# Kernel optimization log

Measured on AMD Instinct MI355X. Metric: run time of the kernel, lower is better.

The kernel has to match this reference:

```python
import jax, jax.numpy as jnp
import numpy as np

N_NODES = 50000
N_EDGES = 800000
N_GRAPHS = 512
D = 128
NUM_GIN_LAYERS = 4
BN_EPS = 1e-5


def setup_inputs() -> dict:
    key = jax.random.key(0)
    ks = jax.random.split(key, 10)
    h = jax.random.normal(ks[0], (N_NODES, D), dtype=jnp.float32)
    src = jax.random.randint(ks[1], (N_EDGES,), 0, N_NODES, dtype=jnp.int32)
    dst = jax.random.randint(ks[2], (N_EDGES,), 0, N_NODES, dtype=jnp.int32)
    graph_id = jnp.sort(jax.random.randint(ks[3], (N_NODES,), 0, N_GRAPHS, dtype=jnp.int32))
    scale = 1.0 / np.sqrt(D)
    W1s = jax.random.normal(ks[4], (NUM_GIN_LAYERS, D, D), dtype=jnp.float32) * scale
    W2s = jax.random.normal(ks[5], (NUM_GIN_LAYERS, D, D), dtype=jnp.float32) * scale
    bn1_g = jnp.ones((NUM_GIN_LAYERS, D), jnp.float32)
    bn1_b = jnp.zeros((NUM_GIN_LAYERS, D), jnp.float32)
    bn2_g = jnp.ones((NUM_GIN_LAYERS, D), jnp.float32)
    bn2_b = jnp.zeros((NUM_GIN_LAYERS, D), jnp.float32)
    pred_W = jax.random.normal(ks[6], (NUM_GIN_LAYERS + 1, D, D), dtype=jnp.float32) * scale
    pred_b = jnp.zeros((NUM_GIN_LAYERS + 1, D), jnp.float32)
    return {"h": h, "src": src, "dst": dst, "graph_id": graph_id,
            "W1s": W1s, "W2s": W2s, "bn1_g": bn1_g, "bn1_b": bn1_b,
            "bn2_g": bn2_g, "bn2_b": bn2_b, "pred_W": pred_W, "pred_b": pred_b}


def _batch_norm(x, gamma, beta):
    # training-mode BN over the node axis
    mean = jnp.mean(x, axis=0)
    var = jnp.var(x, axis=0)
    return (x - mean) * jax.lax.rsqrt(var + BN_EPS) * gamma + beta


def reference(h, src, dst, graph_id, W1s, W2s, bn1_g, bn1_b, bn2_g, bn2_b, pred_W, pred_b):
    n = h.shape[0]
    hidden_rep = [h]
    for i in range(NUM_GIN_LAYERS):
        # GINConv, eps=0: (1+eps)*h + sum over in-neighbors (scatter-sum over edges)
        agg = jax.ops.segment_sum(h[src], dst, num_segments=n)
        z = h + agg
        # two-layer MLP: Linear(no bias) -> BN -> ReLU -> Linear(no bias)
        z = jax.nn.relu(_batch_norm(z @ W1s[i], bn1_g[i], bn1_b[i]))
        z = z @ W2s[i]
        # outer BN + ReLU
        h = jax.nn.relu(_batch_norm(z, bn2_g[i], bn2_b[i]))
        hidden_rep.append(h)
    # graph readout: per-graph max pool over each layer's representation,
    # then per-layer linear prediction summed (dropout is identity in eval)
    score = jnp.zeros((N_GRAPHS, pred_W.shape[-1]), h.dtype)
    for i, hr in enumerate(hidden_rep):
        pooled = jax.ops.segment_max(hr, graph_id, num_segments=N_GRAPHS,
                                     indices_are_sorted=True)
        score = score + pooled @ pred_W[i] + pred_b[i]
    return score
```

## Files before the change

### kernel.cpp

```cpp
#include <hip/hip_runtime.h>

#define N_NODES 50000
#define N_EDGES 800000
#define N_GRAPHS 512
#define DIM 128
#define NLAYERS 4
#define BN_EPS 1e-5f
#define NTILE (N_NODES / 16)
#define POIS ((int)0xAAAAAAAA)
#define NREP 8

#define NBUCK 80
#define CAPB 12288
#define EPB 1600
#define NBIN 500

typedef unsigned short u16;
typedef float f32x2 __attribute__((ext_vector_type(2)));
typedef float f32x4 __attribute__((ext_vector_type(4)));
typedef short bf16x8 __attribute__((ext_vector_type(8)));

__device__ __forceinline__ short f2bs(float f) {
    union { float f; unsigned u; } v; v.f = f;
    unsigned r = v.u + 0x7FFFu + ((v.u >> 16) & 1u);
    return (short)(r >> 16);
}
__device__ __forceinline__ float bu2f(unsigned u) {
    union { unsigned u; float f; } v; v.u = u << 16;
    return v.f;
}
__device__ __forceinline__ unsigned packbf(float x, float y) {
    return ((unsigned)(u16)f2bs(y) << 16) | (unsigned)(u16)f2bs(x);
}

__device__ __forceinline__ void foldbn(const float* __restrict__ st,
                                       const float* __restrict__ gamma,
                                       const float* __restrict__ beta,
                                       float* absm, int tid) {
    if (tid < 128) {
        float s = 0.f, sq = 0.f;
#pragma unroll
        for (int j = 0; j < NREP; j++) {
            s += st[j * 256 + tid];
            sq += st[j * 256 + 128 + tid];
        }
        float mean = s * (1.f / N_NODES);
        float var = sq * (1.f / N_NODES) - mean * mean;
        float a = gamma[tid] * rsqrtf(var + BN_EPS);
        absm[tid] = a;
        absm[DIM + tid] = beta[tid] - mean * a;
    }
}

__global__ __launch_bounds__(256) void k_prepbin(const float* __restrict__ h,
                                                 const float* __restrict__ W1s,
                                                 const float* __restrict__ W2s,
                                                 const int* __restrict__ gid,
                                                 const int* __restrict__ src,
                                                 const int* __restrict__ dst,
                                                 unsigned* __restrict__ hb,
                                                 short* __restrict__ wt,
                                                 int* __restrict__ gs, int* __restrict__ ge,
                                                 unsigned* __restrict__ eb,
                                                 int* __restrict__ gcur) {
    __shared__ int hist[NBUCK], base[NBUCK], lcur[NBUCK];
    int bid = blockIdx.x, tid = threadIdx.x;
    if (bid >= 6250) {
        int bbid = bid - 6250;
        if (tid < NBUCK) hist[tid] = 0;
        __syncthreads();
        int e0 = bbid * EPB;
        unsigned rec[7]; int rb[7];
#pragma unroll
        for (int k = 0; k < 7; k++) {
            int idx = tid + k * 256;
            rb[k] = -1;
            if (idx < EPB) {
                int s = src[e0 + idx], d = dst[e0 + idx];
                rec[k] = ((unsigned)d << 16) | (unsigned)s;
                int x = d / 6250;
                int sub = (d - x * 6250) / 625;
                rb[k] = x + 8 * sub;
                atomicAdd(&hist[rb[k]], 1);
            }
        }
        __syncthreads();
        if (tid < NBUCK) {
            int old = atomicAdd(&gcur[tid], hist[tid]);
            base[tid] = old - POIS;
            lcur[tid] = 0;
        }
        __syncthreads();
#pragma unroll
        for (int k = 0; k < 7; k++) {
            if (rb[k] >= 0) {
                int p = atomicAdd(&lcur[rb[k]], 1);
                eb[rb[k] * CAPB + base[rb[k]] + p] = rec[k];
            }
        }
        return;
    }
    int gtid = bid * 256 + tid;
    {
        f32x4 v = *(const f32x4*)(h + gtid * 4);
        uint2 pp;
        pp.x = packbf(v.x, v.y);
        pp.y = packbf(v.z, v.w);
        *(uint2*)(hb + gtid * 2) = pp;
    }
    if (gtid < 8 * 16384) {
        int m = gtid >> 14, r = gtid & 16383, n = r >> 7, k = r & 127;
        const float* W = (m < 4) ? (W1s + m * 16384) : (W2s + (m - 4) * 16384);
        wt[gtid] = f2bs(W[k * DIM + n]);
    }
    if (gtid < N_NODES) {
        int g = gid[gtid];
        if (gtid == 0 || gid[gtid - 1] != g) gs[g] = gtid;
        if (gtid == N_NODES - 1 || gid[gtid + 1] != g) ge[g] = gtid + 1;
    }
}

__global__ __launch_bounds__(256) void k_fillpool0(const unsigned* __restrict__ eb,
                                                   const int* __restrict__ gcur,
                                                   int* __restrict__ begA,
                                                   int* __restrict__ endA,
                                                   u16* __restrict__ eix,
                                                   const float* __restrict__ h,
                                                   const int* __restrict__ gs,
                                                   const int* __restrict__ ge,
                                                   float* __restrict__ pool4) {
    __shared__ int hist[625], begL[625], sm[256];
    __shared__ f32x2 psm[256];
    int bid = blockIdx.x, tid = threadIdx.x;
    if (bid < NBUCK) {
        int x = bid & 7, sub = bid >> 3;
        int n0 = x * 6250 + sub * 625;
        int mybase = 0, mycnt = 0;
        for (int r = 0; r < NBUCK; r++) {
            int c = gcur[r] - POIS;
            int rx = r & 7, rs = r >> 3;
            if (rx < x || (rx == x && rs < sub)) mybase += c;
            if (r == bid) mycnt = c;
        }
        for (int i = tid; i < 625; i += 256) hist[i] = 0;
        __syncthreads();
        const unsigned* my = eb + bid * CAPB;
        for (int i = tid; i < mycnt; i += 256) {
            int dl = (int)(my[i] >> 16) - n0;
            atomicAdd(&hist[dl], 1);
        }
        __syncthreads();
        int carry = 0;
        for (int c = 0; c < 3; c++) {
            int idx = c * 256 + tid;
            int v = (idx < 625) ? hist[idx] : 0;
            int xv = v;
            sm[tid] = xv; __syncthreads();
#pragma unroll
            for (int d = 1; d < 256; d <<= 1) {
                int y = (tid >= d) ? sm[tid - d] : 0;
                __syncthreads();
                sm[tid] = xv = xv + y;
                __syncthreads();
            }
            if (idx < 625) begL[idx] = mybase + carry + xv - v;
            int ct = sm[255];
            __syncthreads();
            carry += ct;
        }
        __syncthreads();
        for (int i = tid; i < 625; i += 256) {
            int b = begL[i];
            begA[n0 + i] = b;
            endA[n0 + i] = b + hist[i];
        }
        __syncthreads();
        for (int i = tid; i < mycnt; i += 256) {
            unsigned rc = my[i];
            int dl = (int)(rc >> 16) - n0;
            int p = atomicAdd(&begL[dl], 1);
            eix[p] = (u16)(rc & 0xFFFFu);
        }
        return;
    }
    int pb = bid - NBUCK;
    int g = pb >> 2, sub = pb & 3;
    int c2 = (tid & 63) * 2, ro = tid >> 6;
    int beg = gs[g], end = ge[g];
    f32x2 mx = (f32x2){-3.402823e38f, -3.402823e38f};
    if (beg >= 0 && end <= N_NODES) {
        for (int r = beg + sub * 4 + ro; r < end; r += 16) {
            f32x2 v = *(const f32x2*)(h + r * DIM + c2);
            mx.x = fmaxf(mx.x, v.x);
            mx.y = fmaxf(mx.y, v.y);
        }
    }
    psm[tid] = mx;
    __syncthreads();
    if (ro == 0) {
        f32x2 m0 = psm[tid], m1 = psm[tid + 64], m2 = psm[tid + 128], m3 = psm[tid + 192];
        m0.x = fmaxf(fmaxf(m0.x, m1.x), fmaxf(m2.x, m3.x));
        m0.y = fmaxf(fmaxf(m0.y, m1.y), fmaxf(m2.y, m3.y));
        *(f32x2*)(pool4 + pb * DIM + c2) = m0;
    }
}

template <bool XF>
__global__ __launch_bounds__(256) void k_gather(const unsigned* __restrict__ hp,
                                                const int* __restrict__ begA,
                                                const int* __restrict__ endA,
                                                const u16* __restrict__ eix,
                                                const float* __restrict__ absg,
                                                unsigned* __restrict__ Za) {
    int node = blockIdx.x * 4 + (threadIdx.x >> 6);
    int lane = threadIdx.x & 63;
    float a0 = 1.f, a1 = 1.f, b0 = 0.f, b1 = 0.f;
    if (XF) {
        a0 = absg[2 * lane]; a1 = absg[2 * lane + 1];
        b0 = absg[DIM + 2 * lane]; b1 = absg[DIM + 2 * lane + 1];
    }
#define TX(w, rx, ry)                                     \
    {                                                     \
        float _x = bu2f((w) & 0xffffu), _y = bu2f((w) >> 16); \
        if (XF) {                                         \
            _x = fmaxf(a0 * _x + b0, 0.f);                \
            _y = fmaxf(a1 * _y + b1, 0.f);                \
        }                                                 \
        rx += _x; ry += _y;                               \
    }
    float ax = 0.f, ay = 0.f;
    TX(hp[node * 64 + lane], ax, ay);
    int beg = begA[node];
    int end = endA[node];
    int e = beg;
    for (; e + 8 <= end; e += 8) {
        int s0 = eix[e], s1 = eix[e + 1], s2 = eix[e + 2], s3 = eix[e + 3];
        int s4 = eix[e + 4], s5 = eix[e + 5], s6 = eix[e + 6], s7 = eix[e + 7];
        unsigned w0 = hp[s0 * 64 + lane], w1 = hp[s1 * 64 + lane];
        unsigned w2 = hp[s2 * 64 + lane], w3 = hp[s3 * 64 + lane];
        unsigned w4 = hp[s4 * 64 + lane], w5 = hp[s5 * 64 + lane];
        unsigned w6 = hp[s6 * 64 + lane], w7 = hp[s7 * 64 + lane];
        TX(w0, ax, ay); TX(w1, ax, ay); TX(w2, ax, ay); TX(w3, ax, ay);
        TX(w4, ax, ay); TX(w5, ax, ay); TX(w6, ax, ay); TX(w7, ax, ay);
    }
    for (; e < end; e++) {
        unsigned ww = hp[eix[e] * 64 + lane];
        TX(ww, ax, ay);
    }
#undef TX
    Za[node * 64 + lane] = packbf(ax, ay);
}

template <bool XF>
__global__ __launch_bounds__(256, 2) void k_gemm(const unsigned* __restrict__ X,
                                                 const short* __restrict__ wt,
                                                 const float* __restrict__ statsPrev,
                                                 const float* __restrict__ gamma,
                                                 const float* __restrict__ beta,
                                                 unsigned* __restrict__ OUT,
                                                 float* __restrict__ statsDst) {
    __shared__ float tbuf[4][16][68];
    __shared__ float absm[256];
    __shared__ float smst[256];
    const int tid = threadIdx.x, bid = blockIdx.x;
    const int lane = tid & 63, wid = tid >> 6;
    const int ln15 = lane & 15, q = lane >> 4;
    float (*buf)[68] = tbuf[wid];

    bf16x8 bfr[8][4];
#pragma unroll
    for (int tl = 0; tl < 8; tl++)
#pragma unroll
        for (int s = 0; s < 4; s++)
            bfr[tl][s] = *(const bf16x8*)(wt + (tl * 16 + ln15) * DIM + s * 32 + q * 8);

    if (XF) foldbn(statsPrev, gamma, beta, absm, tid);
    smst[tid] = 0.f;
    __syncthreads();

    float sac[8], qac[8];
#pragma unroll
    for (int t = 0; t < 8; t++) { sac[t] = 0.f; qac[t] = 0.f; }

    f32x4 aA[4], aB[4], bA[4], bB[4];
    if (XF) {
#pragma unroll
        for (int s = 0; s < 4; s++) {
            int k0 = s * 32 + q * 8;
            aA[s] = *(const f32x4*)(absm + k0);
            aB[s] = *(const f32x4*)(absm + k0 + 4);
            bA[s] = *(const f32x4*)(absm + DIM + k0);
            bB[s] = *(const f32x4*)(absm + DIM + k0 + 4);
        }
    }

    for (int tile = bid * 4 + wid; tile < NTILE; tile += gridDim.x * 4) {
        const unsigned* xr = X + (tile * 16 + ln15) * 64;
        bf16x8 afr[4];
        if constexpr (!XF) {
#pragma unroll
            for (int s = 0; s < 4; s++)
                afr[s] = *(const bf16x8*)(xr + s * 16 + q * 4);
        } else {
#pragma unroll
            for (int s = 0; s < 4; s++) {
                uint4 wv = *(const uint4*)(xr + s * 16 + q * 4);
                float v0 = fmaxf(aA[s].x * bu2f(wv.x & 0xffffu) + bA[s].x, 0.f);
                float v1 = fmaxf(aA[s].y * bu2f(wv.x >> 16) + bA[s].y, 0.f);
                float v2 = fmaxf(aA[s].z * bu2f(wv.y & 0xffffu) + bA[s].z, 0.f);
                float v3 = fmaxf(aA[s].w * bu2f(wv.y >> 16) + bA[s].w, 0.f);
                float v4 = fmaxf(aB[s].x * bu2f(wv.z & 0xffffu) + bB[s].x, 0.f);
                float v5 = fmaxf(aB[s].y * bu2f(wv.z >> 16) + bB[s].y, 0.f);
                float v6 = fmaxf(aB[s].z * bu2f(wv.w & 0xffffu) + bB[s].z, 0.f);
                float v7 = fmaxf(aB[s].w * bu2f(wv.w >> 16) + bB[s].w, 0.f);
                bf16x8 a;
                a[0] = f2bs(v0); a[1] = f2bs(v1); a[2] = f2bs(v2); a[3] = f2bs(v3);
                a[4] = f2bs(v4); a[5] = f2bs(v5); a[6] = f2bs(v6); a[7] = f2bs(v7);
                afr[s] = a;
            }
        }
        f32x4 acc[8];
#pragma unroll
        for (int t = 0; t < 8; t++) acc[t] = (f32x4){0.f, 0.f, 0.f, 0.f};
#pragma unroll
        for (int s = 0; s < 4; s++) {
#pragma unroll
            for (int t = 0; t < 8; t++)
                acc[t] = __builtin_amdgcn_mfma_f32_16x16x32_bf16(afr[s], bfr[t][s], acc[t], 0, 0, 0);
        }
#pragma unroll
        for (int t = 0; t < 8; t++) {
            float s_l = 0.f, q_l = 0.f;
#pragma unroll
            for (int r = 0; r < 4; r++) {
                float v = acc[t][r];
                s_l += v;
                q_l += v * v;
            }
            s_l += __shfl_xor(s_l, 16); s_l += __shfl_xor(s_l, 32);
            q_l += __shfl_xor(q_l, 16); q_l += __shfl_xor(q_l, 32);
            sac[t] += s_l;
            qac[t] += q_l;
        }
#pragma unroll
        for (int ch = 0; ch < 2; ch++) {
#pragma unroll
            for (int t2 = 0; t2 < 4; t2++) {
                int t = ch * 4 + t2;
#pragma unroll
                for (int r = 0; r < 4; r++)
                    buf[q * 4 + r][t2 * 16 + ln15] = acc[t][r];
            }
#pragma unroll
            for (int rr = 0; rr < 4; rr++) {
                int lr = rr * 4 + q;
                f32x4 v = *(const f32x4*)&buf[lr][ln15 * 4];
                uint2 pp;
                pp.x = packbf(v.x, v.y);
                pp.y = packbf(v.z, v.w);
                *(uint2*)(OUT + (tile * 16 + lr) * 64 + ch * 32 + ln15 * 2) = pp;
            }
        }
    }
    if (lane < 16) {
#pragma unroll
        for (int t = 0; t < 8; t++) {
            atomicAdd(&smst[t * 16 + ln15], sac[t]);
            atomicAdd(&smst[128 + t * 16 + ln15], qac[t]);
        }
    }
    __syncthreads();
    atomicAdd(statsDst + (bid & (NREP - 1)) * 256 + tid, smst[tid]);
}

__global__ __launch_bounds__(256) void k_pool(const unsigned* __restrict__ Zr,
                                              const float* __restrict__ stats,
                                              const float* __restrict__ gamma,
                                              const float* __restrict__ beta,
                                              const int* __restrict__ gs,
                                              const int* __restrict__ ge,
                                              float* __restrict__ pool4,
                                              float* __restrict__ absg) {
    __shared__ float absm[256];
    __shared__ f32x2 psm[256];
    int bid = blockIdx.x, tid = threadIdx.x;
    int g = bid >> 2, sub = bid & 3;
    foldbn(stats, gamma, beta, absm, tid);
    __syncthreads();
    if (bid == 0) absg[tid] = absm[tid];
    int ci = tid & 63, ro = tid >> 6;
    int beg = gs[g], end = ge[g];
    f32x2 a = *(const f32x2*)(absm + ci * 2);
    f32x2 b = *(const f32x2*)(absm + DIM + ci * 2);
    f32x2 mx = (f32x2){-3.402823e38f, -3.402823e38f};
    if (beg >= 0 && end <= N_NODES) {
        for (int r = beg + sub * 4 + ro; r < end; r += 16) {
            unsigned w = Zr[r * 64 + ci];
            float vx = fmaxf(a.x * bu2f(w & 0xffffu) + b.x, 0.f);
            float vy = fmaxf(a.y * bu2f(w >> 16) + b.y, 0.f);
            mx.x = fmaxf(mx.x, vx);
            mx.y = fmaxf(mx.y, vy);
        }
    }
    psm[tid] = mx;
    __syncthreads();
    if (ro == 0) {
        f32x2 m0 = psm[tid], m1 = psm[tid + 64], m2 = psm[tid + 128], m3 = psm[tid + 192];
        m0.x = fmaxf(fmaxf(m0.x, m1.x), fmaxf(m2.x, m3.x));
        m0.y = fmaxf(fmaxf(m0.y, m1.y), fmaxf(m2.y, m3.y));
        *(f32x2*)(pool4 + bid * DIM + ci * 2) = m0;
    }
}

__global__ __launch_bounds__(640) void k_readout(const float* __restrict__ pool4,
                                                 const float* __restrict__ predW,
                                                 const float* __restrict__ predb,
                                                 float* __restrict__ out) {
    __shared__ float pl[5][DIM];
    __shared__ float ps[5][DIM];
    int g = blockIdx.x, t = threadIdx.x;
    int l = t >> 7, c = t & 127;
    {
        const float* p = pool4 + l * (N_GRAPHS * 4 * DIM) + g * 4 * DIM + c;
        float m = fmaxf(fmaxf(p[0], p[DIM]), fmaxf(p[2 * DIM], p[3 * DIM]));
        pl[l][c] = m;
    }
    __syncthreads();
    float acc = 0.f;
    const float* W = predW + l * DIM * DIM;
    const float* prow = pl[l];
#pragma unroll 8
    for (int k = 0; k < DIM; k++) acc += prow[k] * W[k * DIM + c];
    ps[l][c] = acc;
    __syncthreads();
    if (t < DIM) {
        float s = 0.f;
#pragma unroll
        for (int ll = 0; ll < 5; ll++) s += ps[ll][c] + predb[ll * DIM + c];
        out[g * DIM + c] = s;
    }
}

extern "C" void kernel_launch(void* const* d_in, const int* in_sizes, int n_in,
                              void* d_out, int out_size, void* d_ws, size_t ws_size,
                              hipStream_t stream) {
    const float* h_in = (const float*)d_in[0];
    const int* src = (const int*)d_in[1];
    const int* dst = (const int*)d_in[2];
    const int* gid = (const int*)d_in[3];
    const float* W1s = (const float*)d_in[4];
    const float* W2s = (const float*)d_in[5];
    const float* bn1g = (const float*)d_in[6];
    const float* bn1b = (const float*)d_in[7];
    const float* bn2g = (const float*)d_in[8];
    const float* bn2b = (const float*)d_in[9];
    const float* predW = (const float*)d_in[10];
    const float* predb = (const float*)d_in[11];

    char* ws = (char*)d_ws;
    unsigned* hb = (unsigned*)(ws);
    unsigned* Za = (unsigned*)(ws + 12800000);
    unsigned* Yb = (unsigned*)(ws + 25600000);
    unsigned* Zr = (unsigned*)(ws + 38400000);
    short* wt = (short*)(ws + 51200000);
    float* stats = (float*)(ws + 51462144);
    float* pool4 = (float*)(ws + 51527680);
    int* begA = (int*)(ws + 56770560);
    int* endA = (int*)(ws + 56970560);
    u16* eix = (u16*)(ws + 57372800);
    int* gs = (int*)(ws + 60572800);
    int* ge = (int*)(ws + 60574848);
    float* absg = (float*)(ws + 60576896);
    unsigned* eb = (unsigned*)(ws + 25600000);
    int* gcur = (int*)(ws + 25600000 + 8388608);
    float* out = (float*)d_out;

    const int PSTRIDE = N_GRAPHS * 4 * DIM;

    k_prepbin<<<6750, 256, 0, stream>>>(h_in, W1s, W2s, gid, src, dst, hb, wt, gs, ge, eb, gcur);
    k_fillpool0<<<NBUCK + 2048, 256, 0, stream>>>(eb, gcur, begA, endA, eix, h_in, gs, ge, pool4);

    for (int l = 0; l < NLAYERS; l++) {
        if (l == 0)
            k_gather<false><<<12500, 256, 0, stream>>>(hb, begA, endA, eix, absg, Za);
        else
            k_gather<true><<<12500, 256, 0, stream>>>(Zr, begA, endA, eix, absg, Za);
        k_gemm<false><<<512, 256, 0, stream>>>(Za, wt + l * 16384, nullptr, nullptr, nullptr,
                                               Yb, stats + (l * 2) * (NREP * 256));
        k_gemm<true><<<512, 256, 0, stream>>>(Yb, wt + (4 + l) * 16384,
                                              stats + (l * 2) * (NREP * 256), bn1g + l * DIM,
                                              bn1b + l * DIM, Zr,
                                              stats + (l * 2 + 1) * (NREP * 256));
        k_pool<<<2048, 256, 0, stream>>>(Zr, stats + (l * 2 + 1) * (NREP * 256),
                                         bn2g + l * DIM, bn2b + l * DIM, gs, ge,
                                         pool4 + (l + 1) * PSTRIDE, absg);
    }
    k_readout<<<512, 640, 0, stream>>>(pool4, predW, predb, out);
}
```

Measured before the change: 488.3 us.

## Fuse per-layer max-pool into next layer's gather kernel and prefetch GEMM input tiles

The max-pool for layers 0-2 now runs inside the following layer's gather kernel, through extra blocks in one launch. This removes three kernel launches and the absg round trip, and each gather block recomputes the BN fold itself. The GEMM kernels get a fixed tile assignment with register double-buffering, loading the next tile's A fragment before computing the current one to hide global load latency. The stats buffer also moves to a new workspace offset.

```diff
diff --git a/kernel.cpp b/kernel.cpp
--- a/kernel.cpp
+++ b/kernel.cpp
@@ -205,30 +205,18 @@
     }
 }
 
-template <bool XF>
-__global__ __launch_bounds__(256) void k_gather(const unsigned* __restrict__ hp,
-                                                const int* __restrict__ begA,
-                                                const int* __restrict__ endA,
-                                                const u16* __restrict__ eix,
-                                                const float* __restrict__ absg,
-                                                unsigned* __restrict__ Za) {
+__global__ __launch_bounds__(256) void k_gather0(const unsigned* __restrict__ hp,
+                                                 const int* __restrict__ begA,
+                                                 const int* __restrict__ endA,
+                                                 const u16* __restrict__ eix,
+                                                 unsigned* __restrict__ Za) {
     int node = blockIdx.x * 4 + (threadIdx.x >> 6);
     int lane = threadIdx.x & 63;
-    float a0 = 1.f, a1 = 1.f, b0 = 0.f, b1 = 0.f;
-    if (XF) {
-        a0 = absg[2 * lane]; a1 = absg[2 * lane + 1];
-        b0 = absg[DIM + 2 * lane]; b1 = absg[DIM + 2 * lane + 1];
-    }
-#define TX(w, rx, ry)                                     \
-    {                                                     \
-        float _x = bu2f((w) & 0xffffu), _y = bu2f((w) >> 16); \
-        if (XF) {                                         \
-            _x = fmaxf(a0 * _x + b0, 0.f);                \
-            _y = fmaxf(a1 * _y + b1, 0.f);                \
-        }                                                 \
-        rx += _x; ry += _y;                               \
-    }
     float ax = 0.f, ay = 0.f;
+#define TX(w, rx, ry)                                         \
+    {                                                         \
+        rx += bu2f((w) & 0xffffu); ry += bu2f((w) >> 16);     \
+    }
     TX(hp[node * 64 + lane], ax, ay);
     int beg = begA[node];
     int end = endA[node];
@@ -245,6 +233,82 @@
     }
     for (; e < end; e++) {
         unsigned ww = hp[eix[e] * 64 + lane];
+        TX(ww, ax, ay);
+    }
+#undef TX
+    Za[node * 64 + lane] = packbf(ax, ay);
+}
+
+__global__ __launch_bounds__(256) void k_poolgather(const unsigned* __restrict__ Zr,
+                                                    const float* __restrict__ stats,
+                                                    const float* __restrict__ gamma,
+                                                    const float* __restrict__ beta,
+                                                    const int* __restrict__ gs,
+                                                    const int* __restrict__ ge,
+                                                    float* __restrict__ pool4,
+                                                    const int* __restrict__ begA,
+                                                    const int* __restrict__ endA,
+                                                    const u16* __restrict__ eix,
+                                                    unsigned* __restrict__ Za) {
+    __shared__ float absm[256];
+    __shared__ f32x2 psm[256];
+    int bid = blockIdx.x, tid = threadIdx.x;
+    foldbn(stats, gamma, beta, absm, tid);
+    __syncthreads();
+    if (bid < 2048) {
+        int g = bid >> 2, sub = bid & 3;
+        int ci = tid & 63, ro = tid >> 6;
+        int beg = gs[g], end = ge[g];
+        f32x2 a = *(const f32x2*)(absm + ci * 2);
+        f32x2 b = *(const f32x2*)(absm + DIM + ci * 2);
+        f32x2 mx = (f32x2){-3.402823e38f, -3.402823e38f};
+        if (beg >= 0 && end <= N_NODES) {
+            for (int r = beg + sub * 4 + ro; r < end; r += 16) {
+                unsigned w = Zr[r * 64 + ci];
+                float vx = fmaxf(a.x * bu2f(w & 0xffffu) + b.x, 0.f);
+                float vy = fmaxf(a.y * bu2f(w >> 16) + b.y, 0.f);
+                mx.x = fmaxf(mx.x, vx);
+                mx.y = fmaxf(mx.y, vy);
+            }
+        }
+        psm[tid] = mx;
+        __syncthreads();
+        if (ro == 0) {
+            f32x2 m0 = psm[tid], m1 = psm[tid + 64], m2 = psm[tid + 128], m3 = psm[tid + 192];
+            m0.x = fmaxf(fmaxf(m0.x, m1.x), fmaxf(m2.x, m3.x));
+            m0.y = fmaxf(fmaxf(m0.y, m1.y), fmaxf(m2.y, m3.y));
+            *(f32x2*)(pool4 + bid * DIM + ci * 2) = m0;
+        }
+        return;
+    }
+    int node = (bid - 2048) * 4 + (tid >> 6);
+    int lane = tid & 63;
+    float a0 = absm[2 * lane], a1 = absm[2 * lane + 1];
+    float b0 = absm[DIM + 2 * lane], b1 = absm[DIM + 2 * lane + 1];
+#define TX(w, rx, ry)                                         \
+    {                                                         \
+        float _x = bu2f((w) & 0xffffu), _y = bu2f((w) >> 16); \
+        _x = fmaxf(a0 * _x + b0, 0.f);                        \
+        _y = fmaxf(a1 * _y + b1, 0.f);                        \
+        rx += _x; ry += _y;                                   \
+    }
+    float ax = 0.f, ay = 0.f;
+    TX(Zr[node * 64 + lane], ax, ay);
+    int beg = begA[node];
+    int end = endA[node];
+    int e = beg;
+    for (; e + 8 <= end; e += 8) {
+        int s0 = eix[e], s1 = eix[e + 1], s2 = eix[e + 2], s3 = eix[e + 3];
+        int s4 = eix[e + 4], s5 = eix[e + 5], s6 = eix[e + 6], s7 = eix[e + 7];
+        unsigned w0 = Zr[s0 * 64 + lane], w1 = Zr[s1 * 64 + lane];
+        unsigned w2 = Zr[s2 * 64 + lane], w3 = Zr[s3 * 64 + lane];
+        unsigned w4 = Zr[s4 * 64 + lane], w5 = Zr[s5 * 64 + lane];
+        unsigned w6 = Zr[s6 * 64 + lane], w7 = Zr[s7 * 64 + lane];
+        TX(w0, ax, ay); TX(w1, ax, ay); TX(w2, ax, ay); TX(w3, ax, ay);
+        TX(w4, ax, ay); TX(w5, ax, ay); TX(w6, ax, ay); TX(w7, ax, ay);
+    }
+    for (; e < end; e++) {
+        unsigned ww = Zr[eix[e] * 64 + lane];
         TX(ww, ax, ay);
     }
 #undef TX
@@ -294,25 +358,37 @@
         }
     }
 
-    for (int tile = bid * 4 + wid; tile < NTILE; tile += gridDim.x * 4) {
+    int tile = bid + 512 * wid;
+    uint4 wv[4];
+    if (tile < NTILE) {
         const unsigned* xr = X + (tile * 16 + ln15) * 64;
+#pragma unroll
+        for (int s = 0; s < 4; s++) wv[s] = *(const uint4*)(xr + s * 16 + q * 4);
+    }
+    while (tile < NTILE) {
+        int nt = tile + 2048;
+        uint4 nwv[4];
+        if (nt < NTILE) {
+            const unsigned* xr2 = X + (nt * 16 + ln15) * 64;
+#pragma unroll
+            for (int s = 0; s < 4; s++) nwv[s] = *(const uint4*)(xr2 + s * 16 + q * 4);
+        }
         bf16x8 afr[4];
         if constexpr (!XF) {
 #pragma unroll
-            for (int s = 0; s < 4; s++)
-                afr[s] = *(const bf16x8*)(xr + s * 16 + q * 4);
+            for (int s = 0; s < 4; s++) afr[s] = *(bf16x8*)&wv[s];
         } else {
 #pragma unroll
             for (int s = 0; s < 4; s++) {
-                uint4 wv = *(const uint4*)(xr + s * 16 + q * 4);
-                float v0 = fmaxf(aA[s].x * bu2f(wv.x & 0xffffu) + bA[s].x, 0.f);
-                float v1 = fmaxf(aA[s].y * bu2f(wv.x >> 16) + bA[s].y, 0.f);
-                float v2 = fmaxf(aA[s].z * bu2f(wv.y & 0xffffu) + bA[s].z, 0.f);
-                float v3 = fmaxf(aA[s].w * bu2f(wv.y >> 16) + bA[s].w, 0.f);
-                float v4 = fmaxf(aB[s].x * bu2f(wv.z & 0xffffu) + bB[s].x, 0.f);
-                float v5 = fmaxf(aB[s].y * bu2f(wv.z >> 16) + bB[s].y, 0.f);
-                float v6 = fmaxf(aB[s].z * bu2f(wv.w & 0xffffu) + bB[s].z, 0.f);
-                float v7 = fmaxf(aB[s].w * bu2f(wv.w >> 16) + bB[s].w, 0.f);
+                uint4 w4v = wv[s];
+                float v0 = fmaxf(aA[s].x * bu2f(w4v.x & 0xffffu) + bA[s].x, 0.f);
+                float v1 = fmaxf(aA[s].y * bu2f(w4v.x >> 16) + bA[s].y, 0.f);
+                float v2 = fmaxf(aA[s].z * bu2f(w4v.y & 0xffffu) + bA[s].z, 0.f);
+                float v3 = fmaxf(aA[s].w * bu2f(w4v.y >> 16) + bA[s].w, 0.f);
+                float v4 = fmaxf(aB[s].x * bu2f(w4v.z & 0xffffu) + bB[s].x, 0.f);
+                float v5 = fmaxf(aB[s].y * bu2f(w4v.z >> 16) + bB[s].y, 0.f);
+                float v6 = fmaxf(aB[s].z * bu2f(w4v.w & 0xffffu) + bB[s].z, 0.f);
+                float v7 = fmaxf(aB[s].w * bu2f(w4v.w >> 16) + bB[s].w, 0.f);
                 bf16x8 a;
                 a[0] = f2bs(v0); a[1] = f2bs(v1); a[2] = f2bs(v2); a[3] = f2bs(v3);
                 a[4] = f2bs(v4); a[5] = f2bs(v5); a[6] = f2bs(v6); a[7] = f2bs(v7);
@@ -361,6 +437,9 @@
                 *(uint2*)(OUT + (tile * 16 + lr) * 64 + ch * 32 + ln15 * 2) = pp;
             }
         }
+        tile = nt;
+#pragma unroll
+        for (int s = 0; s < 4; s++) wv[s] = nwv[s];
     }
     if (lane < 16) {
 #pragma unroll
@@ -379,15 +458,13 @@
                                               const float* __restrict__ beta,
                                               const int* __restrict__ gs,
                                               const int* __restrict__ ge,
-                                              float* __restrict__ pool4,
-                                              float* __restrict__ absg) {
+                                              float* __restrict__ pool4) {
     __shared__ float absm[256];
     __shared__ f32x2 psm[256];
     int bid = blockIdx.x, tid = threadIdx.x;
     int g = bid >> 2, sub = bid & 3;
     foldbn(stats, gamma, beta, absm, tid);
     __syncthreads();
-    if (bid == 0) absg[tid] = absm[tid];
     int ci = tid & 63, ro = tid >> 6;
     int beg = gs[g], end = ge[g];
     f32x2 a = *(const f32x2*)(absm + ci * 2);
@@ -463,14 +540,13 @@
     unsigned* Yb = (unsigned*)(ws + 25600000);
     unsigned* Zr = (unsigned*)(ws + 38400000);
     short* wt = (short*)(ws + 51200000);
-    float* stats = (float*)(ws + 51462144);
     float* pool4 = (float*)(ws + 51527680);
     int* begA = (int*)(ws + 56770560);
     int* endA = (int*)(ws + 56970560);
     u16* eix = (u16*)(ws + 57372800);
     int* gs = (int*)(ws + 60572800);
     int* ge = (int*)(ws + 60574848);
-    float* absg = (float*)(ws + 60576896);
+    float* stats = (float*)(ws + 60577920);
     unsigned* eb = (unsigned*)(ws + 25600000);
     int* gcur = (int*)(ws + 25600000 + 8388608);
     float* out = (float*)d_out;
@@ -480,20 +556,24 @@
     k_prepbin<<<6750, 256, 0, stream>>>(h_in, W1s, W2s, gid, src, dst, hb, wt, gs, ge, eb, gcur);
     k_fillpool0<<<NBUCK + 2048, 256, 0, stream>>>(eb, gcur, begA, endA, eix, h_in, gs, ge, pool4);
 
-    for (int l = 0; l < NLAYERS; l++) {
-        if (l == 0)
-            k_gather<false><<<12500, 256, 0, stream>>>(hb, begA, endA, eix, absg, Za);
-        else
-            k_gather<true><<<12500, 256, 0, stream>>>(Zr, begA, endA, eix, absg, Za);
+    k_gather0<<<12500, 256, 0, stream>>>(hb, begA, endA, eix, Za);
+    k_gemm<false><<<512, 256, 0, stream>>>(Za, wt + 0 * 16384, nullptr, nullptr, nullptr,
+                                           Yb, stats + 0 * (NREP * 256));
+    k_gemm<true><<<512, 256, 0, stream>>>(Yb, wt + 4 * 16384, stats + 0 * (NREP * 256),
+                                          bn1g, bn1b, Zr, stats + 1 * (NREP * 256));
+    for (int l = 1; l < NLAYERS; l++) {
+        k_poolgather<<<14548, 256, 0, stream>>>(Zr, stats + ((l - 1) * 2 + 1) * (NREP * 256),
+                                                bn2g + (l - 1) * DIM, bn2b + (l - 1) * DIM,
+                                                gs, ge, pool4 + l * PSTRIDE,
+                                                begA, endA, eix, Za);
         k_gemm<false><<<512, 256, 0, stream>>>(Za, wt + l * 16384, nullptr, nullptr, nullptr,
                                                Yb, stats + (l * 2) * (NREP * 256));
         k_gemm<true><<<512, 256, 0, stream>>>(Yb, wt + (4 + l) * 16384,
                                               stats + (l * 2) * (NREP * 256), bn1g + l * DIM,
                                               bn1b + l * DIM, Zr,
                                               stats + (l * 2 + 1) * (NREP * 256));
-        k_pool<<<2048, 256, 0, stream>>>(Zr, stats + (l * 2 + 1) * (NREP * 256),
-                                         bn2g + l * DIM, bn2b + l * DIM, gs, ge,
-                                         pool4 + (l + 1) * PSTRIDE, absg);
-    }
+    }
+    k_pool<<<2048, 256, 0, stream>>>(Zr, stats + 7 * (NREP * 256), bn2g + 3 * DIM,
+                                     bn2b + 3 * DIM, gs, ge, pool4 + 4 * PSTRIDE);
     k_readout<<<512, 640, 0, stream>>>(pool4, predW, predb, out);
 }
```

New measurement: 485.0 us. Within noise of the previous version (-0.7%).
